# Kernel tuning notes

Hardware: AMD Instinct MI355X
Metric: run time of the kernel (lower is better)

## Reference

```python
import jax, jax.numpy as jnp
import numpy as np

IN_DIM = 512        # cfg.hidden_channels
NUM_H_PATCH = 16    # cfg.num_h_patch (v_dim); also k dim after split
BASE = 10000.0      # cfg.base
OUT_DIM = IN_DIM * 2 * NUM_H_PATCH


def setup_inputs() -> dict:
    key = jax.random.key(0)
    k1, k2, k3 = jax.random.split(key, 3)
    b, n = 16, 256
    token = jax.random.normal(k1, (b, n, IN_DIM), dtype=jnp.float32)
    W_proj = jax.random.normal(k2, (IN_DIM, OUT_DIM), dtype=jnp.float32) * (IN_DIM ** -0.5)
    b_proj = jax.random.normal(k3, (OUT_DIM,), dtype=jnp.float32) * 0.01
    return {"token": token, "W_proj": W_proj, "b_proj": b_proj}


def reference(token, W_proj, b_proj):
    b, n, _ = token.shape
    d = 2 * NUM_H_PATCH
    kv = token @ W_proj + b_proj                       # [b, n, in_dim*2*num_h_patch]
    kv = kv.reshape(b, n, IN_DIM, d).transpose(0, 2, 1, 3)  # b h n d, h=in_dim
    k = kv[..., : NUM_H_PATCH]                         # [b, h, n, num_h_patch]
    v = kv[..., NUM_H_PATCH:]                          # [b, h, n, num_h_patch]
    k = jax.nn.silu(k)
    # rotary phase: theta buffer (h, 1, num_h_patch//2), index = n-1-arange(n)
    d_theta = IN_DIM * NUM_H_PATCH
    freqs = BASE ** (-2.0 / d_theta * jnp.arange(d_theta // 2, dtype=jnp.float32))
    theta = freqs.reshape(IN_DIM, 1, NUM_H_PATCH // 2)
    index = (n - 1 - jnp.arange(n, dtype=jnp.float32)).reshape(n, 1)
    ang = theta * index                                # [h, n, num_h_patch//2]
    ang = jnp.repeat(ang, 2, axis=-1)                  # '... d -> ... (d g)', g=2
    cos, sin = jnp.cos(ang), jnp.sin(ang)
    # rotate-half: interleave (-k_odd, k_even)
    k_half = jnp.stack([-k[..., 1::2], k[..., ::2]], axis=-1).reshape(k.shape)
    k = k * cos + k_half * sin
    # fast-weight memory: per-head outer-product reduction over sequence
    wm = jnp.einsum('bhnd,bhne->bdeh', k, v)           # [b, num_h_patch, num_h_patch, in_dim]
    return wm.reshape(b, NUM_H_PATCH * NUM_H_PATCH, IN_DIM)
```

## Files before the change

### kernel.cpp

```cpp
#include <hip/hip_runtime.h>
#include <hip/hip_bf16.h>

typedef __bf16 bf16;
typedef __bf16 bf16x4 __attribute__((ext_vector_type(4)));
typedef __bf16 bf16x8 __attribute__((ext_vector_type(8)));
typedef float f32x4 __attribute__((ext_vector_type(4)));

#define GLOBAL_AS __attribute__((address_space(1)))
#define LDS_AS __attribute__((address_space(3)))

__device__ __forceinline__ void gload_lds16(const void* g, void* l) {
  __builtin_amdgcn_global_load_lds((const GLOBAL_AS void*)g, (LDS_AS void*)l, 16, 0, 0);
}
#define WAITV(n) asm volatile("s_waitcnt vmcnt(" #n ")" ::: "memory")

__global__ __launch_bounds__(256) void pack_a_k(const float* __restrict__ t,
                                                bf16* __restrict__ o) {
  int g = blockIdx.x * 4 + (threadIdx.x >> 6);
  int lane = threadIdx.x & 63;
  int mf = g & 3, wr = (g >> 2) & 3, kb = (g >> 4) & 15, b = g >> 8;
  int m = (b << 8) + (wr << 6) + (mf << 4) + (lane & 15);
  int k = (kb << 5) + ((lane >> 4) << 3);
  const float* src = t + (size_t)m * 512 + k;
  f32x4 v0 = *(const f32x4*)src;
  f32x4 v1 = *(const f32x4*)(src + 4);
  bf16x8 p;
  p[0] = (bf16)v0[0]; p[1] = (bf16)v0[1]; p[2] = (bf16)v0[2]; p[3] = (bf16)v0[3];
  p[4] = (bf16)v1[0]; p[5] = (bf16)v1[1]; p[6] = (bf16)v1[2]; p[7] = (bf16)v1[3];
  *(bf16x8*)(o + ((size_t)g << 9) + (lane << 3)) = p;
}

__global__ __launch_bounds__(256) void pack_b_k(const float* __restrict__ wsrc,
                                                bf16* __restrict__ o) {
  __shared__ float tile[32][65];
  int tileid = blockIdx.x;
  int kb = tileid & 15, jg = tileid >> 4;
  int k0 = kb << 5, j0 = jg << 6;
  int tid = threadIdx.x;
  {
    int r = tid >> 3, c8 = (tid & 7) << 3;
    const float* src = wsrc + (size_t)(k0 + r) * 16384 + j0 + c8;
    f32x4 a = *(const f32x4*)src;
    f32x4 b2 = *(const f32x4*)(src + 4);
    *(f32x4*)&tile[r][c8] = a;
    *(f32x4*)&tile[r][c8 + 4] = b2;
  }
  __syncthreads();
  int lr = tid & 15, khi = (tid >> 4) & 3, nf = tid >> 6;
  int j = (nf << 4) + lr, kk = khi << 3;
  bf16x8 p;
#pragma unroll
  for (int e = 0; e < 8; ++e) p[e] = (bf16)tile[kk + e][j];
  *(bf16x8*)(o + ((size_t)(((jg << 4) + kb) * 4 + nf) << 9) + ((tid & 63) << 3)) = p;
}

__global__ __launch_bounds__(512, 4) void fused_main_k(
    const bf16* __restrict__ Ap, const bf16* __restrict__ Bp,
    const float* __restrict__ bias, float* __restrict__ out) {
  __shared__ char smem[65536];
  const int tid = threadIdx.x;
  const int lane = tid & 63;
  const int w = tid >> 6;
  const int wr = w >> 1;
  const int wc = w & 1;
  const int b = blockIdx.y;
  const int hg = blockIdx.x;
  const int j0 = hg << 7;

  const bf16* Abase = Ap + ((size_t)(b * 16) << 13);
  const bf16* Bbase = Bp + ((size_t)((hg * 2 + wc) * 16) << 11);

  f32x4 acc[4][4] = {};
  bf16x8 bfA[4], bfB[4];

#define LOAD_BFR(dst_, kb_) do { \
    const bf16* p_ = Bbase + ((kb_) * 2048) + (lane << 3); \
    dst_[0] = *(const bf16x8*)(p_);        \
    dst_[1] = *(const bf16x8*)(p_ + 512);  \
    dst_[2] = *(const bf16x8*)(p_ + 1024); \
    dst_[3] = *(const bf16x8*)(p_ + 1536); \
  } while (0)
#define STAGE_A(kb_, buf_) do { \
    gload_lds16(Abase + ((size_t)(kb_) << 13) + (tid << 3), \
                smem + (buf_) * 16384 + tid * 16); \
    gload_lds16(Abase + ((size_t)(kb_) << 13) + ((tid + 512) << 3), \
                smem + (buf_) * 16384 + (tid + 512) * 16); \
  } while (0)

  LOAD_BFR(bfA, 0);
  STAGE_A(0, 0);
  STAGE_A(1, 1);
  WAITV(2);
  __builtin_amdgcn_s_barrier();
  asm volatile("" ::: "memory");

#pragma unroll
  for (int t = 0; t < 16; ++t) {
    const int cb = (t % 3) * 16384;
    if (t < 15) { if (t & 1) LOAD_BFR(bfA, t + 1); else LOAD_BFR(bfB, t + 1); }
    if (t < 14) STAGE_A(t + 2, (t + 2) % 3);
    bf16x8 af[4];
#pragma unroll
    for (int mf = 0; mf < 4; ++mf)
      af[mf] = *(const bf16x8*)(smem + cb + ((wr * 4 + mf) << 10) + (lane << 4));
    __builtin_amdgcn_s_setprio(1);
#pragma unroll
    for (int mf = 0; mf < 4; ++mf)
#pragma unroll
      for (int nf = 0; nf < 4; ++nf)
        acc[mf][nf] = __builtin_amdgcn_mfma_f32_16x16x32_bf16(
            af[mf], (t & 1) ? bfB[nf] : bfA[nf], acc[mf][nf], 0, 0, 0);
    __builtin_amdgcn_s_setprio(0);
    asm volatile("" ::: "memory");
    if (t < 14) { WAITV(2); } else { WAITV(0); }
    __builtin_amdgcn_s_barrier();
    asm volatile("" ::: "memory");
  }
#undef LOAD_BFR
#undef STAGE_A

#pragma unroll
  for (int nf = 0; nf < 4; ++nf) {
    const int col = wc * 64 + nf * 16 + (lane & 15);
    const int hl = col >> 5;
    const int dd = lane & 15;
    const bool isk = ((nf & 1) == 0);
    const float bv = bias[j0 + col];
    float freq = 0.f, sgn = 0.f;
    if (isk) {
      const int tp = dd >> 1;
      const int hglob = (hg << 2) + hl;
      freq = exp2f((float)(hglob * 8 + tp) * (-13.287712379549449f / 4096.0f));
      sgn = (dd & 1) ? 1.0f : -1.0f;
    }
#pragma unroll
    for (int mf = 0; mf < 4; ++mf) {
      const int n0 = wr * 64 + mf * 16 + ((lane >> 4) << 2);
      f32x4 c = acc[mf][nf];
#pragma unroll
      for (int j = 0; j < 4; ++j) {
        float x = c[j] + bv;
        if (isk) x = x * __builtin_amdgcn_rcpf(1.0f + __expf(-x));
        c[j] = x;
      }
      if (isk) {
#pragma unroll
        for (int j = 0; j < 4; ++j) {
          float partner = __shfl_xor(c[j], 1);
          float sv, cv;
          __sincosf(freq * (float)(255 - (n0 + j)), &sv, &cv);
          c[j] = c[j] * cv + sgn * partner * sv;
        }
      }
      bf16x4 pk;
      pk[0] = (bf16)c[0]; pk[1] = (bf16)c[1]; pk[2] = (bf16)c[2]; pk[3] = (bf16)c[3];
      int byte = (isk ? 0 : 32768) + hl * 8192 + dd * 512 + n0 * 2;
      byte ^= ((dd & 7) << 4);
      *(bf16x4*)(smem + byte) = pk;
    }
  }
  __syncthreads();

  {
    const int hl = w >> 1;
    const int half = w & 1;
    const int dd = lane & 15;
    f32x4 d2 = {0.f, 0.f, 0.f, 0.f};
#pragma unroll
    for (int kk = 0; kk < 4; ++kk) {
      const int n0 = half * 128 + kk * 32 + ((lane >> 4) << 3);
      int byte = hl * 8192 + dd * 512 + n0 * 2;
      byte ^= ((dd & 7) << 4);
      bf16x8 ka = *(const bf16x8*)(smem + byte);
      bf16x8 vb = *(const bf16x8*)(smem + 32768 + byte);
      d2 = __builtin_amdgcn_mfma_f32_16x16x32_bf16(ka, vb, d2, 0, 0, 0);
    }
    __syncthreads();
    float* part = (float*)smem;
#pragma unroll
    for (int j = 0; j < 4; ++j) {
      int de = (((lane >> 4) << 2) + j) * 16 + dd;
      part[w * 256 + de] = d2[j];
    }
  }
  __syncthreads();

  if (tid < 256) {
    const float* part = (const float*)smem;
    f32x4 o;
#pragma unroll
    for (int hl = 0; hl < 4; ++hl)
      o[hl] = part[(2 * hl) * 256 + tid] + part[(2 * hl + 1) * 256 + tid];
    *(f32x4*)(out + (size_t)b * 131072 + (size_t)tid * 512 + hg * 4) = o;
  }
}

extern "C" void kernel_launch(void* const* d_in, const int* in_sizes, int n_in,
                              void* d_out, int out_size, void* d_ws, size_t ws_size,
                              hipStream_t stream) {
  const float* token = (const float*)d_in[0];
  const float* W     = (const float*)d_in[1];
  const float* bias  = (const float*)d_in[2];
  float* out = (float*)d_out;

  bf16* Apack = (bf16*)d_ws;
  bf16* Bpack = (bf16*)((char*)d_ws + (size_t)4 * 1024 * 1024);

  pack_a_k<<<1024, 256, 0, stream>>>(token, Apack);
  pack_b_k<<<4096, 256, 0, stream>>>(W, Bpack);
  fused_main_k<<<dim3(128, 16), 512, 0, stream>>>(Apack, Bpack, bias, out);
}
```

Baseline: 96.35 us.

## Use 256-thread blocks with larger per-wave tiles and LDS-staged B double buffering

```diff
diff --git a/kernel.cpp b/kernel.cpp
--- a/kernel.cpp
+++ b/kernel.cpp
@@ -12,14 +12,13 @@
 __device__ __forceinline__ void gload_lds16(const void* g, void* l) {
   __builtin_amdgcn_global_load_lds((const GLOBAL_AS void*)g, (LDS_AS void*)l, 16, 0, 0);
 }
-#define WAITV(n) asm volatile("s_waitcnt vmcnt(" #n ")" ::: "memory")
 
 __global__ __launch_bounds__(256) void pack_a_k(const float* __restrict__ t,
                                                 bf16* __restrict__ o) {
   int g = blockIdx.x * 4 + (threadIdx.x >> 6);
   int lane = threadIdx.x & 63;
-  int mf = g & 3, wr = (g >> 2) & 3, kb = (g >> 4) & 15, b = g >> 8;
-  int m = (b << 8) + (wr << 6) + (mf << 4) + (lane & 15);
+  int mf = g & 3, rg = (g >> 2) & 3, kb = (g >> 4) & 15, b = g >> 8;
+  int m = (b << 8) + (rg << 6) + (mf << 4) + (lane & 15);
   int k = (kb << 5) + ((lane >> 4) << 3);
   const float* src = t + (size_t)m * 512 + k;
   f32x4 v0 = *(const f32x4*)src;
@@ -54,74 +53,66 @@
   *(bf16x8*)(o + ((size_t)(((jg << 4) + kb) * 4 + nf) << 9) + ((tid & 63) << 3)) = p;
 }
 
-__global__ __launch_bounds__(512, 4) void fused_main_k(
+__global__ __launch_bounds__(256, 2) void fused_main_k(
     const bf16* __restrict__ Ap, const bf16* __restrict__ Bp,
     const float* __restrict__ bias, float* __restrict__ out) {
   __shared__ char smem[65536];
   const int tid = threadIdx.x;
   const int lane = tid & 63;
   const int w = tid >> 6;
-  const int wr = w >> 1;
-  const int wc = w & 1;
+  const int wm = w >> 1;
+  const int wn = w & 1;
   const int b = blockIdx.y;
   const int hg = blockIdx.x;
   const int j0 = hg << 7;
 
-  const bf16* Abase = Ap + ((size_t)(b * 16) << 13);
-  const bf16* Bbase = Bp + ((size_t)((hg * 2 + wc) * 16) << 11);
-
-  f32x4 acc[4][4] = {};
-  bf16x8 bfA[4], bfB[4];
-
-#define LOAD_BFR(dst_, kb_) do { \
-    const bf16* p_ = Bbase + ((kb_) * 2048) + (lane << 3); \
-    dst_[0] = *(const bf16x8*)(p_);        \
-    dst_[1] = *(const bf16x8*)(p_ + 512);  \
-    dst_[2] = *(const bf16x8*)(p_ + 1024); \
-    dst_[3] = *(const bf16x8*)(p_ + 1536); \
+  const bf16* Abase = Ap + ((size_t)b << 17);
+
+  f32x4 acc[8][4] = {};
+
+#define STAGE(t_, d_) do { \
+    _Pragma("unroll") \
+    for (int i_ = 0; i_ < 4; ++i_) { \
+      int c_ = i_ * 256 + tid; \
+      gload_lds16(Abase + ((size_t)(t_) << 13) + (c_ << 3), \
+                  smem + (d_) * 24576 + (c_ << 4)); \
+    } \
+    _Pragma("unroll") \
+    for (int j_ = 0; j_ < 2; ++j_) { \
+      gload_lds16(Bp + (((size_t)(2 * hg + j_) * 16 + (t_)) << 11) + (tid << 3), \
+                  smem + (d_) * 24576 + 16384 + j_ * 4096 + (tid << 4)); \
+    } \
   } while (0)
-#define STAGE_A(kb_, buf_) do { \
-    gload_lds16(Abase + ((size_t)(kb_) << 13) + (tid << 3), \
-                smem + (buf_) * 16384 + tid * 16); \
-    gload_lds16(Abase + ((size_t)(kb_) << 13) + ((tid + 512) << 3), \
-                smem + (buf_) * 16384 + (tid + 512) * 16); \
-  } while (0)
-
-  LOAD_BFR(bfA, 0);
-  STAGE_A(0, 0);
-  STAGE_A(1, 1);
-  WAITV(2);
-  __builtin_amdgcn_s_barrier();
-  asm volatile("" ::: "memory");
+
+  STAGE(0, 0);
+  __syncthreads();
 
 #pragma unroll
   for (int t = 0; t < 16; ++t) {
-    const int cb = (t % 3) * 16384;
-    if (t < 15) { if (t & 1) LOAD_BFR(bfA, t + 1); else LOAD_BFR(bfB, t + 1); }
-    if (t < 14) STAGE_A(t + 2, (t + 2) % 3);
-    bf16x8 af[4];
-#pragma unroll
-    for (int mf = 0; mf < 4; ++mf)
-      af[mf] = *(const bf16x8*)(smem + cb + ((wr * 4 + mf) << 10) + (lane << 4));
+    const int d = (t & 1) * 24576;
+    if (t < 15) STAGE(t + 1, (t + 1) & 1);
+    bf16x8 af[8], bfr[4];
+#pragma unroll
+    for (int mf = 0; mf < 8; ++mf)
+      af[mf] = *(const bf16x8*)(smem + d + ((wm * 8 + mf) << 10) + (lane << 4));
+#pragma unroll
+    for (int nf = 0; nf < 4; ++nf)
+      bfr[nf] = *(const bf16x8*)(smem + d + 16384 + ((wn * 4 + nf) << 10) + (lane << 4));
     __builtin_amdgcn_s_setprio(1);
 #pragma unroll
-    for (int mf = 0; mf < 4; ++mf)
+    for (int mf = 0; mf < 8; ++mf)
 #pragma unroll
       for (int nf = 0; nf < 4; ++nf)
         acc[mf][nf] = __builtin_amdgcn_mfma_f32_16x16x32_bf16(
-            af[mf], (t & 1) ? bfB[nf] : bfA[nf], acc[mf][nf], 0, 0, 0);
+            af[mf], bfr[nf], acc[mf][nf], 0, 0, 0);
     __builtin_amdgcn_s_setprio(0);
-    asm volatile("" ::: "memory");
-    if (t < 14) { WAITV(2); } else { WAITV(0); }
-    __builtin_amdgcn_s_barrier();
-    asm volatile("" ::: "memory");
-  }
-#undef LOAD_BFR
-#undef STAGE_A
+    __syncthreads();
+  }
+#undef STAGE
 
 #pragma unroll
   for (int nf = 0; nf < 4; ++nf) {
-    const int col = wc * 64 + nf * 16 + (lane & 15);
+    const int col = wn * 64 + nf * 16 + (lane & 15);
     const int hl = col >> 5;
     const int dd = lane & 15;
     const bool isk = ((nf & 1) == 0);
@@ -134,8 +125,8 @@
       sgn = (dd & 1) ? 1.0f : -1.0f;
     }
 #pragma unroll
-    for (int mf = 0; mf < 4; ++mf) {
-      const int n0 = wr * 64 + mf * 16 + ((lane >> 4) << 2);
+    for (int mf = 0; mf < 8; ++mf) {
+      const int n0 = wm * 128 + (mf >> 2) * 64 + (mf & 3) * 16 + ((lane >> 4) << 2);
       f32x4 c = acc[mf][nf];
 #pragma unroll
       for (int j = 0; j < 4; ++j) {
@@ -162,14 +153,12 @@
   __syncthreads();
 
   {
-    const int hl = w >> 1;
-    const int half = w & 1;
     const int dd = lane & 15;
     f32x4 d2 = {0.f, 0.f, 0.f, 0.f};
 #pragma unroll
-    for (int kk = 0; kk < 4; ++kk) {
-      const int n0 = half * 128 + kk * 32 + ((lane >> 4) << 3);
-      int byte = hl * 8192 + dd * 512 + n0 * 2;
+    for (int kk = 0; kk < 8; ++kk) {
+      const int n0 = kk * 32 + ((lane >> 4) << 3);
+      int byte = w * 8192 + dd * 512 + n0 * 2;
       byte ^= ((dd & 7) << 4);
       bf16x8 ka = *(const bf16x8*)(smem + byte);
       bf16x8 vb = *(const bf16x8*)(smem + 32768 + byte);
@@ -185,12 +174,11 @@
   }
   __syncthreads();
 
-  if (tid < 256) {
+  {
     const float* part = (const float*)smem;
     f32x4 o;
 #pragma unroll
-    for (int hl = 0; hl < 4; ++hl)
-      o[hl] = part[(2 * hl) * 256 + tid] + part[(2 * hl + 1) * 256 + tid];
+    for (int ch = 0; ch < 4; ++ch) o[ch] = part[ch * 256 + tid];
     *(f32x4*)(out + (size_t)b * 131072 + (size_t)tid * 512 + hg * 4) = o;
   }
 }
@@ -208,5 +196,5 @@
 
   pack_a_k<<<1024, 256, 0, stream>>>(token, Apack);
   pack_b_k<<<4096, 256, 0, stream>>>(W, Bpack);
-  fused_main_k<<<dim3(128, 16), 512, 0, stream>>>(Apack, Bpack, bias, out);
-}
+  fused_main_k<<<dim3(128, 16), 256, 0, stream>>>(Apack, Bpack, bias, out);
+}
```

Result: slower. 99.62 us (+3.4%).

## Switch GEMM to 32x32x16 MFMA with B staged through LDS

Applied to the files above, without the earlier changes.

```diff
diff --git a/kernel.cpp b/kernel.cpp
--- a/kernel.cpp
+++ b/kernel.cpp
@@ -5,6 +5,7 @@
 typedef __bf16 bf16x4 __attribute__((ext_vector_type(4)));
 typedef __bf16 bf16x8 __attribute__((ext_vector_type(8)));
 typedef float f32x4 __attribute__((ext_vector_type(4)));
+typedef float f32x16 __attribute__((ext_vector_type(16)));
 
 #define GLOBAL_AS __attribute__((address_space(1)))
 #define LDS_AS __attribute__((address_space(3)))
@@ -14,50 +15,60 @@
 }
 #define WAITV(n) asm volatile("s_waitcnt vmcnt(" #n ")" ::: "memory")
 
-__global__ __launch_bounds__(256) void pack_a_k(const float* __restrict__ t,
+__global__ __launch_bounds__(256) void pack_a_k(const float* __restrict__ tok,
                                                 bf16* __restrict__ o) {
-  int g = blockIdx.x * 4 + (threadIdx.x >> 6);
-  int lane = threadIdx.x & 63;
-  int mf = g & 3, wr = (g >> 2) & 3, kb = (g >> 4) & 15, b = g >> 8;
-  int m = (b << 8) + (wr << 6) + (mf << 4) + (lane & 15);
-  int k = (kb << 5) + ((lane >> 4) << 3);
-  const float* src = t + (size_t)m * 512 + k;
-  f32x4 v0 = *(const f32x4*)src;
-  f32x4 v1 = *(const f32x4*)(src + 4);
+  __shared__ float tile[64][33];
+  int bid = blockIdx.x;
+  int t = bid & 15, wr = (bid >> 4) & 3, b = bid >> 6;
+  int tid = threadIdx.x;
+  {
+    int r = tid >> 2, kc = (tid & 3) << 3;
+    const float* src = tok + (size_t)(b * 256 + wr * 64 + r) * 512 + t * 32 + kc;
+    f32x4 a = *(const f32x4*)src;
+    f32x4 c = *(const f32x4*)(src + 4);
+    *(f32x4*)&tile[r][kc] = a;
+    *(f32x4*)&tile[r][kc + 4] = c;
+  }
+  __syncthreads();
+  int lane = tid & 63, fc = tid >> 6;
+  int mi = fc >> 1, kh = fc & 1;
   bf16x8 p;
-  p[0] = (bf16)v0[0]; p[1] = (bf16)v0[1]; p[2] = (bf16)v0[2]; p[3] = (bf16)v0[3];
-  p[4] = (bf16)v1[0]; p[5] = (bf16)v1[1]; p[6] = (bf16)v1[2]; p[7] = (bf16)v1[3];
-  *(bf16x8*)(o + ((size_t)g << 9) + (lane << 3)) = p;
+#pragma unroll
+  for (int e = 0; e < 8; ++e)
+    p[e] = (bf16)tile[mi * 32 + (lane & 31)][kh * 16 + ((lane >> 5) << 3) + e];
+  *(bf16x8*)(o + ((size_t)(b * 16 + t) * 16 + (wr * 4 + fc)) * 512 + (lane << 3)) = p;
 }
 
 __global__ __launch_bounds__(256) void pack_b_k(const float* __restrict__ wsrc,
                                                 bf16* __restrict__ o) {
   __shared__ float tile[32][65];
-  int tileid = blockIdx.x;
-  int kb = tileid & 15, jg = tileid >> 4;
-  int k0 = kb << 5, j0 = jg << 6;
+  int bid = blockIdx.x;
+  int t = bid & 15, jg = bid >> 4;
   int tid = threadIdx.x;
   {
     int r = tid >> 3, c8 = (tid & 7) << 3;
-    const float* src = wsrc + (size_t)(k0 + r) * 16384 + j0 + c8;
+    const float* src = wsrc + (size_t)(t * 32 + r) * 16384 + jg * 64 + c8;
     f32x4 a = *(const f32x4*)src;
-    f32x4 b2 = *(const f32x4*)(src + 4);
+    f32x4 c = *(const f32x4*)(src + 4);
     *(f32x4*)&tile[r][c8] = a;
-    *(f32x4*)&tile[r][c8 + 4] = b2;
-  }
-  __syncthreads();
-  int lr = tid & 15, khi = (tid >> 4) & 3, nf = tid >> 6;
-  int j = (nf << 4) + lr, kk = khi << 3;
+    *(f32x4*)&tile[r][c8 + 4] = c;
+  }
+  __syncthreads();
+  int lane = tid & 63, fc = tid >> 6;
+  int cgl = fc >> 1, kh = fc & 1;
   bf16x8 p;
 #pragma unroll
-  for (int e = 0; e < 8; ++e) p[e] = (bf16)tile[kk + e][j];
-  *(bf16x8*)(o + ((size_t)(((jg << 4) + kb) * 4 + nf) << 9) + ((tid & 63) << 3)) = p;
+  for (int e = 0; e < 8; ++e)
+    p[e] = (bf16)tile[kh * 16 + ((lane >> 5) << 3) + e][cgl * 32 + (lane & 31)];
+  int hg = jg >> 1, half = jg & 1;
+  int fB = (half * 2 + cgl) * 2 + kh;
+  *(bf16x8*)(o + ((size_t)(hg * 16 + t) * 8 + fB) * 512 + (lane << 3)) = p;
 }
 
 __global__ __launch_bounds__(512, 4) void fused_main_k(
     const bf16* __restrict__ Ap, const bf16* __restrict__ Bp,
     const float* __restrict__ bias, float* __restrict__ out) {
-  __shared__ char smem[65536];
+  __shared__ char smem[73728];
   const int tid = threadIdx.x;
   const int lane = tid & 63;
   const int w = tid >> 6;
@@ -67,96 +78,106 @@
   const int hg = blockIdx.x;
   const int j0 = hg << 7;
 
-  const bf16* Abase = Ap + ((size_t)(b * 16) << 13);
-  const bf16* Bbase = Bp + ((size_t)((hg * 2 + wc) * 16) << 11);
-
-  f32x4 acc[4][4] = {};
-  bf16x8 bfA[4], bfB[4];
-
-#define LOAD_BFR(dst_, kb_) do { \
-    const bf16* p_ = Bbase + ((kb_) * 2048) + (lane << 3); \
-    dst_[0] = *(const bf16x8*)(p_);        \
-    dst_[1] = *(const bf16x8*)(p_ + 512);  \
-    dst_[2] = *(const bf16x8*)(p_ + 1024); \
-    dst_[3] = *(const bf16x8*)(p_ + 1536); \
+  const bf16* Abase = Ap + ((size_t)b << 17);
+  const bf16* Bbase = Bp + ((size_t)hg << 16);
+
+  f32x16 acc[2][2] = {};
+
+#define STAGE(t_, buf_) do { \
+    gload_lds16(Abase + ((size_t)(t_) << 13) + (tid << 3), \
+                smem + (buf_) * 24576 + tid * 16); \
+    gload_lds16(Abase + ((size_t)(t_) << 13) + ((tid + 512) << 3), \
+                smem + (buf_) * 24576 + (tid + 512) * 16); \
+    gload_lds16(Bbase + ((size_t)(t_) << 12) + (tid << 3), \
+                smem + (buf_) * 24576 + 16384 + tid * 16); \
   } while (0)
-#define STAGE_A(kb_, buf_) do { \
-    gload_lds16(Abase + ((size_t)(kb_) << 13) + (tid << 3), \
-                smem + (buf_) * 16384 + tid * 16); \
-    gload_lds16(Abase + ((size_t)(kb_) << 13) + ((tid + 512) << 3), \
-                smem + (buf_) * 16384 + (tid + 512) * 16); \
-  } while (0)
-
-  LOAD_BFR(bfA, 0);
-  STAGE_A(0, 0);
-  STAGE_A(1, 1);
-  WAITV(2);
+
+  STAGE(0, 0);
+  STAGE(1, 1);
+  WAITV(3);
   __builtin_amdgcn_s_barrier();
   asm volatile("" ::: "memory");
 
 #pragma unroll
   for (int t = 0; t < 16; ++t) {
-    const int cb = (t % 3) * 16384;
-    if (t < 15) { if (t & 1) LOAD_BFR(bfA, t + 1); else LOAD_BFR(bfB, t + 1); }
-    if (t < 14) STAGE_A(t + 2, (t + 2) % 3);
-    bf16x8 af[4];
-#pragma unroll
-    for (int mf = 0; mf < 4; ++mf)
-      af[mf] = *(const bf16x8*)(smem + cb + ((wr * 4 + mf) << 10) + (lane << 4));
+    const int cb = (t % 3) * 24576;
+    if (t < 14) STAGE(t + 2, (t + 2) % 3);
+    bf16x8 af[2][2], bf[2][2];
+#pragma unroll
+    for (int mi = 0; mi < 2; ++mi)
+#pragma unroll
+      for (int kh = 0; kh < 2; ++kh)
+        af[mi][kh] = *(const bf16x8*)(smem + cb +
+            ((wr * 4 + mi * 2 + kh) << 10) + (lane << 4));
+#pragma unroll
+    for (int ni = 0; ni < 2; ++ni)
+#pragma unroll
+      for (int kh = 0; kh < 2; ++kh)
+        bf[ni][kh] = *(const bf16x8*)(smem + cb + 16384 +
+            (((wc * 2 + ni) * 2 + kh) << 10) + (lane << 4));
     __builtin_amdgcn_s_setprio(1);
 #pragma unroll
-    for (int mf = 0; mf < 4; ++mf)
-#pragma unroll
-      for (int nf = 0; nf < 4; ++nf)
-        acc[mf][nf] = __builtin_amdgcn_mfma_f32_16x16x32_bf16(
-            af[mf], (t & 1) ? bfB[nf] : bfA[nf], acc[mf][nf], 0, 0, 0);
+    for (int kh = 0; kh < 2; ++kh)
+#pragma unroll
+      for (int mi = 0; mi < 2; ++mi)
+#pragma unroll
+        for (int ni = 0; ni < 2; ++ni)
+          acc[mi][ni] = __builtin_amdgcn_mfma_f32_32x32x16_bf16(
+              af[mi][kh], bf[ni][kh], acc[mi][ni], 0, 0, 0);
     __builtin_amdgcn_s_setprio(0);
     asm volatile("" ::: "memory");
-    if (t < 14) { WAITV(2); } else { WAITV(0); }
+    if (t < 14) { WAITV(3); } else if (t == 14) { WAITV(0); }
     __builtin_amdgcn_s_barrier();
     asm volatile("" ::: "memory");
   }
-#undef LOAD_BFR
-#undef STAGE_A
-
-#pragma unroll
-  for (int nf = 0; nf < 4; ++nf) {
-    const int col = wc * 64 + nf * 16 + (lane & 15);
-    const int hl = col >> 5;
+#undef STAGE
+
+  {
+    const int d31 = lane & 31;
     const int dd = lane & 15;
-    const bool isk = ((nf & 1) == 0);
-    const float bv = bias[j0 + col];
-    float freq = 0.f, sgn = 0.f;
-    if (isk) {
-      const int tp = dd >> 1;
-      const int hglob = (hg << 2) + hl;
-      freq = exp2f((float)(hglob * 8 + tp) * (-13.287712379549449f / 4096.0f));
-      sgn = (dd & 1) ? 1.0f : -1.0f;
-    }
-#pragma unroll
-    for (int mf = 0; mf < 4; ++mf) {
-      const int n0 = wr * 64 + mf * 16 + ((lane >> 4) << 2);
-      f32x4 c = acc[mf][nf];
-#pragma unroll
-      for (int j = 0; j < 4; ++j) {
-        float x = c[j] + bv;
-        if (isk) x = x * __builtin_amdgcn_rcpf(1.0f + __expf(-x));
-        c[j] = x;
+    const bool isk = d31 < 16;
+    const float sgn = (d31 & 1) ? 1.0f : -1.0f;
+#pragma unroll
+    for (int ni = 0; ni < 2; ++ni) {
+      const int hl = wc * 2 + ni;
+      const int col = wc * 64 + ni * 32 + d31;
+      const float bv = bias[j0 + col];
+      float freq = 0.f;
+      if (isk) {
+        const int tp = dd >> 1;
+        const int hglob = (hg << 2) + hl;
+        freq = exp2f((float)(hglob * 8 + tp) * (-13.287712379549449f / 4096.0f));
       }
-      if (isk) {
-#pragma unroll
-        for (int j = 0; j < 4; ++j) {
-          float partner = __shfl_xor(c[j], 1);
-          float sv, cv;
-          __sincosf(freq * (float)(255 - (n0 + j)), &sv, &cv);
-          c[j] = c[j] * cv + sgn * partner * sv;
+#pragma unroll
+      for (int mi = 0; mi < 2; ++mi) {
+        f32x16 c = acc[mi][ni];
+#pragma unroll
+        for (int r = 0; r < 16; ++r) {
+          float x = c[r] + bv;
+          if (isk) x = x * __builtin_amdgcn_rcpf(1.0f + __expf(-x));
+          c[r] = x;
+        }
+        if (isk) {
+#pragma unroll
+          for (int r = 0; r < 16; ++r) {
+            float partner = __shfl_xor(c[r], 1);
+            int n = wr * 64 + mi * 32 + (r & 3) + ((r >> 2) << 3) + ((lane >> 5) << 2);
+            float sv, cv;
+            __sincosf(freq * (float)(255 - n), &sv, &cv);
+            c[r] = c[r] * cv + sgn * partner * sv;
+          }
+        }
+#pragma unroll
+        for (int q = 0; q < 4; ++q) {
+          bf16x4 pk;
+          pk[0] = (bf16)c[q * 4 + 0]; pk[1] = (bf16)c[q * 4 + 1];
+          pk[2] = (bf16)c[q * 4 + 2]; pk[3] = (bf16)c[q * 4 + 3];
+          int n0 = wr * 64 + mi * 32 + (q << 3) + ((lane >> 5) << 2);
+          int byte = (isk ? 0 : 32768) + hl * 8192 + dd * 512 + n0 * 2;
+          byte ^= ((dd & 7) << 4);
+          *(bf16x4*)(smem + byte) = pk;
         }
       }
-      bf16x4 pk;
-      pk[0] = (bf16)c[0]; pk[1] = (bf16)c[1]; pk[2] = (bf16)c[2]; pk[3] = (bf16)c[3];
-      int byte = (isk ? 0 : 32768) + hl * 8192 + dd * 512 + n0 * 2;
-      byte ^= ((dd & 7) << 4);
-      *(bf16x4*)(smem + byte) = pk;
     }
   }
   __syncthreads();
```

New measurement: 112.2 us. 1.16x slower.
